# Kernel tuning notes

Hardware: AMD Instinct MI355X
Metric: run time of the kernel (lower is better)

The kernel has to match this reference:

```python
import jax, jax.numpy as jnp
import numpy as np

N_NODES = 50000
N_EDGES = 800000
IN_FEATS = 128
N_HIDDEN = 128
N_CLASSES = 64


def setup_inputs() -> dict:
    key = jax.random.key(0)
    ks = jax.random.split(key, 12)
    x = jax.random.normal(ks[0], (N_NODES, IN_FEATS), dtype=jnp.float32)
    src = jax.random.randint(ks[1], (N_EDGES,), 0, N_NODES, dtype=jnp.int32)
    dst = jax.random.randint(ks[2], (N_EDGES,), 0, N_NODES, dtype=jnp.int32)
    dims = [(IN_FEATS, N_HIDDEN), (N_HIDDEN, N_HIDDEN), (N_HIDDEN, N_CLASSES)]
    inp = {"x": x, "src": src, "dst": dst}
    for i, (din, dout) in enumerate(dims):
        s = (2.0 / (din + dout)) ** 0.5  # xavier-ish init scale
        inp[f"Wself{i}"] = jax.random.normal(ks[3 + 3 * i], (din, dout), dtype=jnp.float32) * s
        inp[f"Wneigh{i}"] = jax.random.normal(ks[4 + 3 * i], (din, dout), dtype=jnp.float32) * s
        inp[f"b{i}"] = jnp.zeros((dout,), dtype=jnp.float32)
    return inp


def _sage_conv(h, src, dst, inv_deg, Wself, Wneigh, b):
    # mean aggregation over in-neighbors: gather on src, segment-sum on dst
    agg = jax.ops.segment_sum(h[src], dst, num_segments=N_NODES)  # [N, d]
    h_neigh = agg * inv_deg[:, None]
    return h @ Wself + h_neigh @ Wneigh + b


def reference(x, src, dst, Wself0, Wneigh0, b0, Wself1, Wneigh1, b1, Wself2, Wneigh2, b2):
    # in-degree (clamped to 1, matching DGL mean aggregator), shared across layers
    deg = jax.ops.segment_sum(jnp.ones((N_EDGES,), dtype=jnp.float32), dst, num_segments=N_NODES)
    inv_deg = 1.0 / jnp.maximum(deg, 1.0)
    # dropout is identity in eval mode
    h = _sage_conv(x, src, dst, inv_deg, Wself0, Wneigh0, b0)
    h = jax.nn.relu(h)
    h = _sage_conv(h, src, dst, inv_deg, Wself1, Wneigh1, b1)
    h = jax.nn.relu(h)
    h = _sage_conv(h, src, dst, inv_deg, Wself2, Wneigh2, b2)
    return h
```

## Files before the change

### kernel.cpp

```cpp
#include <hip/hip_runtime.h>

#define N_NODES 50000
#define N_EDGES 800000
#define NB_SCAN 196
#define NODES_PER_GRP 6250
#define BUCKET_CAP 131072

typedef unsigned short ushort_t;
typedef __attribute__((ext_vector_type(8))) short  short8v;
typedef __attribute__((ext_vector_type(4))) float  float4v;
typedef __attribute__((ext_vector_type(4))) unsigned short ushort4v;
typedef __attribute__((ext_vector_type(8))) unsigned short ushort8v;
typedef __attribute__((ext_vector_type(4))) int int4v;

__device__ __forceinline__ ushort_t f2bf(float f) {
    unsigned u = __float_as_uint(f);
    unsigned r = 0x7fffu + ((u >> 16) & 1u);
    return (ushort_t)((u + r) >> 16);
}
__device__ __forceinline__ float bf2f(ushort_t h) {
    return __uint_as_float((unsigned)h << 16);
}

__global__ __launch_bounds__(256) void cast_zero_k(const float* __restrict__ x,
                                                   ushort_t* __restrict__ xb,
                                                   int* __restrict__ deg,
                                                   int* __restrict__ bcur, int n4) {
    int i = blockIdx.x * 256 + threadIdx.x;
    if (i < n4) {
        float4 v = ((const float4*)x)[i];
        ushort4v h;
        h[0] = f2bf(v.x); h[1] = f2bf(v.y); h[2] = f2bf(v.z); h[3] = f2bf(v.w);
        ((ushort4v*)xb)[i] = h;
    }
    if (i < N_NODES) deg[i] = 0;
    if (i < 8) bcur[i] = 0;
}

__global__ __launch_bounds__(256) void bucket_k(const int4v* __restrict__ dst4,
                                                const int4v* __restrict__ src4,
                                                int* __restrict__ bcur,
                                                int2* __restrict__ buckets) {
    __shared__ int lcount[8];
    __shared__ int lbase[8];
    const int t = threadIdx.x, b = blockIdx.x;
    if (t < 8) lcount[t] = 0;
    __syncthreads();

    int4v d[4], s[4];
    const int base4 = b * 1024 + t;
#pragma unroll
    for (int i = 0; i < 4; ++i) {
        int idx = base4 + i * 256;
        if (idx < N_EDGES / 4) {
            d[i] = __builtin_nontemporal_load(dst4 + idx);
            s[i] = __builtin_nontemporal_load(src4 + idx);
        } else {
            d[i][0] = d[i][1] = d[i][2] = d[i][3] = -1;
            s[i][0] = s[i][1] = s[i][2] = s[i][3] = 0;
        }
    }
    int g[16], li[16];
#pragma unroll
    for (int i = 0; i < 4; ++i)
#pragma unroll
        for (int j = 0; j < 4; ++j) {
            int e = i * 4 + j;
            int dv = d[i][j];
            g[e] = (dv >= 0) ? (dv / NODES_PER_GRP) : -1;
            li[e] = (g[e] >= 0) ? atomicAdd(&lcount[g[e]], 1) : 0;
        }
    __syncthreads();
    if (t < 8) lbase[t] = atomicAdd(bcur + t, lcount[t]);
    __syncthreads();
#pragma unroll
    for (int i = 0; i < 4; ++i)
#pragma unroll
        for (int j = 0; j < 4; ++j) {
            int e = i * 4 + j;
            if (g[e] >= 0) {
                int pos = lbase[g[e]] + li[e];
                buckets[(size_t)g[e] * BUCKET_CAP + pos] = make_int2(d[i][j], s[i][j]);
            }
        }
}

__global__ __launch_bounds__(256) void deg_bucket_k(const int* __restrict__ bcur,
                                                    const int2* __restrict__ buckets,
                                                    int* __restrict__ deg) {
    const int grp = blockIdx.x & 7;
    const int cnt = bcur[grp];
    const int2* bk = buckets + (size_t)grp * BUCKET_CAP;
    const int stride = (gridDim.x >> 3) * 256;
    for (int i = (blockIdx.x >> 3) * 256 + threadIdx.x; i < cnt; i += stride) {
        atomicAdd(deg + bk[i].x, 1);
    }
}


__global__ __launch_bounds__(256) void block_sum_k(const int* __restrict__ deg,
                                                   int* __restrict__ bsum, int n) {
    __shared__ int s[256];
    int t = threadIdx.x, b = blockIdx.x;
    int i = b * 256 + t;
    s[t] = (i < n) ? deg[i] : 0;
    __syncthreads();
#pragma unroll
    for (int off = 128; off > 0; off >>= 1) {
        if (t < off) s[t] += s[t + off];
        __syncthreads();
    }
    if (t == 0) bsum[b] = s[0];
}

__global__ __launch_bounds__(256) void scan_bsum_k(const int* __restrict__ bsum,
                                                   int* __restrict__ boff,
                                                   int* __restrict__ rowptr_last, int nb) {
    __shared__ int s[256];
    int t = threadIdx.x;
    int v = (t < nb) ? bsum[t] : 0;
    s[t] = v;
    __syncthreads();
#pragma unroll
    for (int off = 1; off < 256; off <<= 1) {
        int u = (t >= off) ? s[t - off] : 0;
        __syncthreads();
        s[t] += u;
        __syncthreads();
    }
    if (t < nb) boff[t] = s[t] - v;
    if (t == 255) *rowptr_last = s[255];
}

__global__ __launch_bounds__(256) void write_rowptr_k(const int* __restrict__ deg,
                                                      const int* __restrict__ boff,
                                                      int* __restrict__ rowptr,
                                                      int* __restrict__ cursor,
                                                      float* __restrict__ inv, int n) {
    __shared__ int s[256];
    int t = threadIdx.x, b = blockIdx.x;
    int i = b * 256 + t;
    int d = (i < n) ? deg[i] : 0;
    s[t] = d;
    __syncthreads();
#pragma unroll
    for (int off = 1; off < 256; off <<= 1) {
        int u = (t >= off) ? s[t - off] : 0;
        __syncthreads();
        s[t] += u;
        __syncthreads();
    }
    if (i < n) {
        int r = boff[b] + s[t] - d;
        rowptr[i] = r;
        cursor[i] = r;
        inv[i] = 1.0f / fmaxf((float)d, 1.0f);
    }
}

__global__ __launch_bounds__(256) void scatter_bucket_k(const int* __restrict__ bcur,
                                                        const int2* __restrict__ buckets,
                                                        int* __restrict__ cursor,
                                                        int* __restrict__ csr) {
    const int grp = blockIdx.x & 7;
    const int cnt = bcur[grp];
    const int2* bk = buckets + (size_t)grp * BUCKET_CAP;
    const int stride = (gridDim.x >> 3) * 256;
    for (int i = (blockIdx.x >> 3) * 256 + threadIdx.x; i < cnt; i += stride) {
        int2 e = bk[i];
        csr[atomicAdd(cursor + e.x, 1)] = e.y;
    }
}

__global__ __launch_bounds__(256) void pack_all_k(const float* __restrict__ W0n, const float* __restrict__ W0s,
                                                  const float* __restrict__ W1n, const float* __restrict__ W1s,
                                                  const float* __restrict__ W2n, const float* __restrict__ W2s,
                                                  ushort_t* __restrict__ P) {
    int tid = blockIdx.x * 256 + threadIdx.x;
    const float* W; int dout; int base; int r;
    if      (tid < 2048)  { W = W0n; dout = 128; base = 0;     r = tid; }
    else if (tid < 4096)  { W = W0s; dout = 128; base = 16384; r = tid - 2048; }
    else if (tid < 6144)  { W = W1n; dout = 128; base = 32768; r = tid - 4096; }
    else if (tid < 8192)  { W = W1s; dout = 128; base = 49152; r = tid - 6144; }
    else if (tid < 9216)  { W = W2n; dout = 64;  base = 65536; r = tid - 8192; }
    else                  { W = W2s; dout = 64;  base = 73728; r = tid - 9216; }
    int lane = r & 63;
    int ks = (r >> 6) & 3;
    int nt = r >> 8;
    int col = nt * 16 + (lane & 15);
    int k0 = ks * 32 + ((lane >> 4) << 3);
    ushort_t* d = P + (size_t)base + (size_t)r * 8;
    ushort4v lo4, hi4;
#pragma unroll
    for (int j = 0; j < 4; ++j) lo4[j] = f2bf(W[(size_t)(k0 + j) * dout + col]);
#pragma unroll
    for (int j = 0; j < 4; ++j) hi4[j] = f2bf(W[(size_t)(k0 + 4 + j) * dout + col]);
    *(ushort4v*)d = lo4;
    *(ushort4v*)(d + 4) = hi4;
}

__global__ __launch_bounds__(256) void aggm_k(const ushort_t* __restrict__ h,
                                              const int* __restrict__ rowptr,
                                              const int* __restrict__ csr,
                                              const float* __restrict__ inv,
                                              ushort_t* __restrict__ m, int N) {
    int node = (blockIdx.x * 256 + threadIdx.x) >> 4;
    int c = threadIdx.x & 15;
    if (node >= N) return;
    int start = rowptr[node], end = rowptr[node + 1];

    const ushort8v* hp = (const ushort8v*)h;
    float a0[8] = {}, a1[8] = {}, a2[8] = {}, a3[8] = {};
    int j = start;
    for (; j + 3 < end; j += 4) {
        int u0 = csr[j], u1 = csr[j + 1], u2 = csr[j + 2], u3 = csr[j + 3];
        ushort8v w0 = hp[(size_t)u0 * 16 + c];
        ushort8v w1 = hp[(size_t)u1 * 16 + c];
        ushort8v w2 = hp[(size_t)u2 * 16 + c];
        ushort8v w3 = hp[(size_t)u3 * 16 + c];
#pragma unroll
        for (int k = 0; k < 8; ++k) {
            a0[k] += bf2f(w0[k]); a1[k] += bf2f(w1[k]);
            a2[k] += bf2f(w2[k]); a3[k] += bf2f(w3[k]);
        }
    }
    for (; j < end; ++j) {
        ushort8v w = hp[(size_t)csr[j] * 16 + c];
#pragma unroll
        for (int k = 0; k < 8; ++k) a0[k] += bf2f(w[k]);
    }
    float s = inv[node];
    ushort8v o;
#pragma unroll
    for (int k = 0; k < 8; ++k) o[k] = f2bf(((a0[k] + a1[k]) + (a2[k] + a3[k])) * s);
    ((ushort8v*)m)[(size_t)node * 16 + c] = o;
}

__global__ __launch_bounds__(256, 4) void fusedgemm_k(const ushort_t* __restrict__ H,
                                                      const ushort_t* __restrict__ M,
                                                      const short8v* __restrict__ Ws,
                                                      const short8v* __restrict__ Wn,
                                                      const float* __restrict__ bias,
                                                      ushort_t* __restrict__ Out, int N) {
    __shared__ ushort_t sm[2][64 * 128];
    char* sbH = (char*)sm[0];
    char* sbM = (char*)sm[1];
    const int bm = blockIdx.x * 64;
    const int t = threadIdx.x;
    const int w = t >> 6, l = t & 63;

    {
        const ushort8v* Hp = (const ushort8v*)H;
        const ushort8v* Mp = (const ushort8v*)M;
        ushort8v zeroV = {0, 0, 0, 0, 0, 0, 0, 0};
#pragma unroll
        for (int it = 0; it < 4; ++it) {
            int r = it * 16 + (t >> 4);
            int row = bm + r;
            int byte = (r * 256 + (t & 15) * 16) ^ ((r & 7) << 4);
            ushort8v vh = zeroV, vm = zeroV;
            if (row < N) {
                vh = Hp[(size_t)row * 16 + (t & 15)];
                vm = Mp[(size_t)row * 16 + (t & 15)];
            }
            *(ushort8v*)(sbH + byte) = vh;
            *(ushort8v*)(sbM + byte) = vm;
        }
    }
    __syncthreads();

    float bv[8];
#pragma unroll
    for (int nt = 0; nt < 8; ++nt) bv[nt] = bias[nt * 16 + (l & 15)];

    float4v acc[8] = {};
#pragma unroll
    for (int ks = 0; ks < 4; ++ks) {
        int r0 = w * 16 + (l & 15);
        int b0 = (r0 * 256 + ks * 64 + (l >> 4) * 16) ^ ((r0 & 7) << 4);
        short8v ah = *(const short8v*)(sbH + b0);
        short8v am = *(const short8v*)(sbM + b0);
#pragma unroll
        for (int nt = 0; nt < 8; ++nt) {
            short8v bs = Ws[(nt * 4 + ks) * 64 + l];
            short8v bn = Wn[(nt * 4 + ks) * 64 + l];
            acc[nt] = __builtin_amdgcn_mfma_f32_16x16x32_bf16(ah, bs, acc[nt], 0, 0, 0);
            acc[nt] = __builtin_amdgcn_mfma_f32_16x16x32_bf16(am, bn, acc[nt], 0, 0, 0);
        }
    }

#pragma unroll
    for (int i = 0; i < 4; ++i) {
        int row = bm + w * 16 + (l >> 4) * 4 + i;
        if (row < N) {
#pragma unroll
            for (int nt = 0; nt < 8; ++nt) {
                int col = nt * 16 + (l & 15);
                Out[(size_t)row * 128 + col] = f2bf(fmaxf(acc[nt][i] + bv[nt], 0.f));
            }
        }
    }
}

__global__ __launch_bounds__(256, 4) void dual64_k(const ushort_t* __restrict__ A,
                                                   const short8v* __restrict__ Wn,
                                                   const short8v* __restrict__ Ws,
                                                   const float* __restrict__ bias,
                                                   ushort_t* __restrict__ Z,
                                                   float* __restrict__ S, int N) {
    constexpr int NT = 4;
    __shared__ ushort_t Asm[64 * 128];
    char* sb = (char*)Asm;
    const int bm = blockIdx.x * 64;
    const int t = threadIdx.x;
    const int w = t >> 6, l = t & 63;

    {
        const ushort8v* Ap = (const ushort8v*)A;
        ushort8v zeroV = {0, 0, 0, 0, 0, 0, 0, 0};
#pragma unroll
        for (int it = 0; it < 4; ++it) {
            int r = it * 16 + (t >> 4);
            int row = bm + r;
            ushort8v v = zeroV;
            if (row < N) v = Ap[(size_t)row * 16 + (t & 15)];
            int byte = (r * 256 + (t & 15) * 16) ^ ((r & 7) << 4);
            *(ushort8v*)(sb + byte) = v;
        }
    }
    __syncthreads();

    float bv[NT];
#pragma unroll
    for (int nt = 0; nt < NT; ++nt) bv[nt] = bias[nt * 16 + (l & 15)];

    float4v accS[NT] = {}, accN[NT] = {};
#pragma unroll
    for (int ks = 0; ks < 4; ++ks) {
        int r0 = w * 16 + (l & 15);
        int b0 = (r0 * 256 + ks * 64 + (l >> 4) * 16) ^ ((r0 & 7) << 4);
        short8v a = *(const short8v*)(sb + b0);
#pragma unroll
        for (int nt = 0; nt < NT; ++nt) {
            short8v bs = Ws[(nt * 4 + ks) * 64 + l];
            short8v bn = Wn[(nt * 4 + ks) * 64 + l];
            accS[nt] = __builtin_amdgcn_mfma_f32_16x16x32_bf16(a, bs, accS[nt], 0, 0, 0);
            accN[nt] = __builtin_amdgcn_mfma_f32_16x16x32_bf16(a, bn, accN[nt], 0, 0, 0);
        }
    }

#pragma unroll
    for (int i = 0; i < 4; ++i) {
        int row = bm + w * 16 + (l >> 4) * 4 + i;
        if (row < N) {
#pragma unroll
            for (int nt = 0; nt < NT; ++nt) {
                int col = nt * 16 + (l & 15);
                S[(size_t)row * 64 + col] = accS[nt][i] + bv[nt];
                Z[(size_t)row * 64 + col] = f2bf(accN[nt][i]);
            }
        }
    }
}

__global__ __launch_bounds__(256) void agg64_k(const ushort_t* __restrict__ z,
                                               const int* __restrict__ rowptr,
                                               const int* __restrict__ csr,
                                               const float* __restrict__ inv,
                                               float* __restrict__ out, int N) {
    int node = (blockIdx.x * 256 + threadIdx.x) >> 3;
    int c = threadIdx.x & 7;
    if (node >= N) return;
    int start = rowptr[node], end = rowptr[node + 1];

    const ushort8v* zp = (const ushort8v*)z;
    float a0[8] = {}, a1[8] = {}, a2[8] = {}, a3[8] = {};
    int j = start;
    for (; j + 3 < end; j += 4) {
        int u0 = csr[j], u1 = csr[j + 1], u2 = csr[j + 2], u3 = csr[j + 3];
        ushort8v w0 = zp[(size_t)u0 * 8 + c];
        ushort8v w1 = zp[(size_t)u1 * 8 + c];
        ushort8v w2 = zp[(size_t)u2 * 8 + c];
        ushort8v w3 = zp[(size_t)u3 * 8 + c];
#pragma unroll
        for (int k = 0; k < 8; ++k) {
            a0[k] += bf2f(w0[k]); a1[k] += bf2f(w1[k]);
            a2[k] += bf2f(w2[k]); a3[k] += bf2f(w3[k]);
        }
    }
    for (; j < end; ++j) {
        ushort8v w = zp[(size_t)csr[j] * 8 + c];
#pragma unroll
        for (int k = 0; k < 8; ++k) a0[k] += bf2f(w[k]);
    }
    float s = inv[node];
    float* op = out + (size_t)node * 64 + c * 8;
    float4 o0 = *(float4*)op;
    float4 o1 = *(float4*)(op + 4);
    o0.x += ((a0[0] + a1[0]) + (a2[0] + a3[0])) * s;
    o0.y += ((a0[1] + a1[1]) + (a2[1] + a3[1])) * s;
    o0.z += ((a0[2] + a1[2]) + (a2[2] + a3[2])) * s;
    o0.w += ((a0[3] + a1[3]) + (a2[3] + a3[3])) * s;
    o1.x += ((a0[4] + a1[4]) + (a2[4] + a3[4])) * s;
    o1.y += ((a0[5] + a1[5]) + (a2[5] + a3[5])) * s;
    o1.z += ((a0[6] + a1[6]) + (a2[6] + a3[6])) * s;
    o1.w += ((a0[7] + a1[7]) + (a2[7] + a3[7])) * s;
    *(float4*)op = o0;
    *(float4*)(op + 4) = o1;
}


extern "C" void kernel_launch(void* const* d_in, const int* in_sizes, int n_in,
                              void* d_out, int out_size, void* d_ws, size_t ws_size,
                              hipStream_t stream) {
    const float* x       = (const float*)d_in[0];
    const int*   src     = (const int*)d_in[1];
    const int*   dst     = (const int*)d_in[2];
    const float* Wself0  = (const float*)d_in[3];
    const float* Wneigh0 = (const float*)d_in[4];
    const float* b0      = (const float*)d_in[5];
    const float* Wself1  = (const float*)d_in[6];
    const float* Wneigh1 = (const float*)d_in[7];
    const float* b1      = (const float*)d_in[8];
    const float* Wself2  = (const float*)d_in[9];
    const float* Wneigh2 = (const float*)d_in[10];
    const float* b2      = (const float*)d_in[11];
    float* out = (float*)d_out;

    char* ws = (char*)d_ws;
    size_t off = 0;
    auto alloc = [&](size_t bytes) -> void* {
        void* p = ws + off;
        off += (bytes + 255) & ~(size_t)255;
        return p;
    };
    int*      deg     = (int*)alloc((size_t)N_NODES * 4);
    float*    inv     = (float*)alloc((size_t)N_NODES * 4);
    int*      rowptr  = (int*)alloc((size_t)(N_NODES + 1) * 4);
    int*      cursor  = (int*)alloc((size_t)N_NODES * 4);
    int*      csr     = (int*)alloc((size_t)N_EDGES * 4);
    int*      bsum    = (int*)alloc((size_t)NB_SCAN * 4);
    int*      boff    = (int*)alloc((size_t)NB_SCAN * 4);
    int*      bcur    = (int*)alloc((size_t)8 * 4);
    int2*     buckets = (int2*)alloc((size_t)8 * BUCKET_CAP * 8);
    ushort_t* packW   = (ushort_t*)alloc((size_t)81920 * 2);
    ushort_t* xb      = (ushort_t*)alloc((size_t)N_NODES * 128 * 2);
    ushort_t* mbuf    = (ushort_t*)alloc((size_t)N_NODES * 128 * 2);
    ushort_t* h1      = (ushort_t*)alloc((size_t)N_NODES * 128 * 2);
    ushort_t* h2      = (ushort_t*)alloc((size_t)N_NODES * 128 * 2);
    ushort_t* z64     = (ushort_t*)alloc((size_t)N_NODES * 64 * 2);

    dim3 b256(256);
    const int gemmBlocks   = (N_NODES + 63) / 64;
    const int aggmBlocks   = (N_NODES * 16 + 255) / 256;
    const int agg64Blocks  = (N_NODES * 8 + 255) / 256;
    const int castBlocks   = (N_NODES * 32 + 255) / 256;
    const int bucketBlocks = (N_EDGES + 4095) / 4096;

    cast_zero_k<<<castBlocks, b256, 0, stream>>>(x, xb, deg, bcur, N_NODES * 32);
    bucket_k<<<bucketBlocks, b256, 0, stream>>>((const int4v*)dst, (const int4v*)src, bcur, buckets);
    deg_bucket_k<<<512, b256, 0, stream>>>(bcur, buckets, deg);
    block_sum_k<<<NB_SCAN, b256, 0, stream>>>(deg, bsum, N_NODES);
    scan_bsum_k<<<1, b256, 0, stream>>>(bsum, boff, rowptr + N_NODES, NB_SCAN);
    write_rowptr_k<<<NB_SCAN, b256, 0, stream>>>(deg, boff, rowptr, cursor, inv, N_NODES);
    scatter_bucket_k<<<512, b256, 0, stream>>>(bcur, buckets, cursor, csr);

    pack_all_k<<<40, b256, 0, stream>>>(Wneigh0, Wself0, Wneigh1, Wself1, Wneigh2, Wself2, packW);
    const short8v* pN0 = (const short8v*)(packW);
    const short8v* pS0 = (const short8v*)(packW + 16384);
    const short8v* pN1 = (const short8v*)(packW + 32768);
    const short8v* pS1 = (const short8v*)(packW + 49152);
    const short8v* pN2 = (const short8v*)(packW + 65536);
    const short8v* pS2 = (const short8v*)(packW + 73728);

    aggm_k<<<aggmBlocks, b256, 0, stream>>>(xb, rowptr, csr, inv, mbuf, N_NODES);
    fusedgemm_k<<<gemmBlocks, b256, 0, stream>>>(xb, mbuf, pS0, pN0, b0, h1, N_NODES);

    aggm_k<<<aggmBlocks, b256, 0, stream>>>(h1, rowptr, csr, inv, mbuf, N_NODES);
    fusedgemm_k<<<gemmBlocks, b256, 0, stream>>>(h1, mbuf, pS1, pN1, b1, h2, N_NODES);

    dual64_k<<<gemmBlocks, b256, 0, stream>>>(h2, pN2, pS2, b2, z64, out, N_NODES);
    agg64_k<<<agg64Blocks, b256, 0, stream>>>(z64, rowptr, csr, inv, out, N_NODES);
}
```

Baseline: 220.5 us.

## Fuse preprocessing kernels to cut launches in CSR build and weight packing

Merges weight packing into the cast kernel via extra blocks, folds degree counting into the bucketing kernel with global atomics on dst, and combines the block-offset scan with the rowptr write so each block redoes the small 196-entry scan. This removes three kernel launches and the extra pass over the bucket buffer. In exchange, bucket_k now issues 800k scattered global atomics inline, and every rowptr block repeats the tiny scan.

```diff
diff --git a/kernel.cpp b/kernel.cpp
--- a/kernel.cpp
+++ b/kernel.cpp
@@ -5,6 +5,7 @@
 #define NB_SCAN 196
 #define NODES_PER_GRP 6250
 #define BUCKET_CAP 131072
+#define CAST_BLOCKS 6250
 
 typedef unsigned short ushort_t;
 typedef __attribute__((ext_vector_type(8))) short  short8v;
@@ -22,161 +23,28 @@
     return __uint_as_float((unsigned)h << 16);
 }
 
-__global__ __launch_bounds__(256) void cast_zero_k(const float* __restrict__ x,
+__global__ __launch_bounds__(256) void cast_pack_k(const float* __restrict__ x,
                                                    ushort_t* __restrict__ xb,
                                                    int* __restrict__ deg,
-                                                   int* __restrict__ bcur, int n4) {
-    int i = blockIdx.x * 256 + threadIdx.x;
-    if (i < n4) {
-        float4 v = ((const float4*)x)[i];
-        ushort4v h;
-        h[0] = f2bf(v.x); h[1] = f2bf(v.y); h[2] = f2bf(v.z); h[3] = f2bf(v.w);
-        ((ushort4v*)xb)[i] = h;
-    }
-    if (i < N_NODES) deg[i] = 0;
-    if (i < 8) bcur[i] = 0;
-}
-
-__global__ __launch_bounds__(256) void bucket_k(const int4v* __restrict__ dst4,
-                                                const int4v* __restrict__ src4,
-                                                int* __restrict__ bcur,
-                                                int2* __restrict__ buckets) {
-    __shared__ int lcount[8];
-    __shared__ int lbase[8];
-    const int t = threadIdx.x, b = blockIdx.x;
-    if (t < 8) lcount[t] = 0;
-    __syncthreads();
-
-    int4v d[4], s[4];
-    const int base4 = b * 1024 + t;
-#pragma unroll
-    for (int i = 0; i < 4; ++i) {
-        int idx = base4 + i * 256;
-        if (idx < N_EDGES / 4) {
-            d[i] = __builtin_nontemporal_load(dst4 + idx);
-            s[i] = __builtin_nontemporal_load(src4 + idx);
-        } else {
-            d[i][0] = d[i][1] = d[i][2] = d[i][3] = -1;
-            s[i][0] = s[i][1] = s[i][2] = s[i][3] = 0;
-        }
-    }
-    int g[16], li[16];
-#pragma unroll
-    for (int i = 0; i < 4; ++i)
-#pragma unroll
-        for (int j = 0; j < 4; ++j) {
-            int e = i * 4 + j;
-            int dv = d[i][j];
-            g[e] = (dv >= 0) ? (dv / NODES_PER_GRP) : -1;
-            li[e] = (g[e] >= 0) ? atomicAdd(&lcount[g[e]], 1) : 0;
-        }
-    __syncthreads();
-    if (t < 8) lbase[t] = atomicAdd(bcur + t, lcount[t]);
-    __syncthreads();
-#pragma unroll
-    for (int i = 0; i < 4; ++i)
-#pragma unroll
-        for (int j = 0; j < 4; ++j) {
-            int e = i * 4 + j;
-            if (g[e] >= 0) {
-                int pos = lbase[g[e]] + li[e];
-                buckets[(size_t)g[e] * BUCKET_CAP + pos] = make_int2(d[i][j], s[i][j]);
-            }
-        }
-}
-
-__global__ __launch_bounds__(256) void deg_bucket_k(const int* __restrict__ bcur,
-                                                    const int2* __restrict__ buckets,
-                                                    int* __restrict__ deg) {
-    const int grp = blockIdx.x & 7;
-    const int cnt = bcur[grp];
-    const int2* bk = buckets + (size_t)grp * BUCKET_CAP;
-    const int stride = (gridDim.x >> 3) * 256;
-    for (int i = (blockIdx.x >> 3) * 256 + threadIdx.x; i < cnt; i += stride) {
-        atomicAdd(deg + bk[i].x, 1);
-    }
-}
-
-
-__global__ __launch_bounds__(256) void block_sum_k(const int* __restrict__ deg,
-                                                   int* __restrict__ bsum, int n) {
-    __shared__ int s[256];
-    int t = threadIdx.x, b = blockIdx.x;
-    int i = b * 256 + t;
-    s[t] = (i < n) ? deg[i] : 0;
-    __syncthreads();
-#pragma unroll
-    for (int off = 128; off > 0; off >>= 1) {
-        if (t < off) s[t] += s[t + off];
-        __syncthreads();
-    }
-    if (t == 0) bsum[b] = s[0];
-}
-
-__global__ __launch_bounds__(256) void scan_bsum_k(const int* __restrict__ bsum,
-                                                   int* __restrict__ boff,
-                                                   int* __restrict__ rowptr_last, int nb) {
-    __shared__ int s[256];
-    int t = threadIdx.x;
-    int v = (t < nb) ? bsum[t] : 0;
-    s[t] = v;
-    __syncthreads();
-#pragma unroll
-    for (int off = 1; off < 256; off <<= 1) {
-        int u = (t >= off) ? s[t - off] : 0;
-        __syncthreads();
-        s[t] += u;
-        __syncthreads();
-    }
-    if (t < nb) boff[t] = s[t] - v;
-    if (t == 255) *rowptr_last = s[255];
-}
-
-__global__ __launch_bounds__(256) void write_rowptr_k(const int* __restrict__ deg,
-                                                      const int* __restrict__ boff,
-                                                      int* __restrict__ rowptr,
-                                                      int* __restrict__ cursor,
-                                                      float* __restrict__ inv, int n) {
-    __shared__ int s[256];
-    int t = threadIdx.x, b = blockIdx.x;
-    int i = b * 256 + t;
-    int d = (i < n) ? deg[i] : 0;
-    s[t] = d;
-    __syncthreads();
-#pragma unroll
-    for (int off = 1; off < 256; off <<= 1) {
-        int u = (t >= off) ? s[t - off] : 0;
-        __syncthreads();
-        s[t] += u;
-        __syncthreads();
-    }
-    if (i < n) {
-        int r = boff[b] + s[t] - d;
-        rowptr[i] = r;
-        cursor[i] = r;
-        inv[i] = 1.0f / fmaxf((float)d, 1.0f);
-    }
-}
-
-__global__ __launch_bounds__(256) void scatter_bucket_k(const int* __restrict__ bcur,
-                                                        const int2* __restrict__ buckets,
-                                                        int* __restrict__ cursor,
-                                                        int* __restrict__ csr) {
-    const int grp = blockIdx.x & 7;
-    const int cnt = bcur[grp];
-    const int2* bk = buckets + (size_t)grp * BUCKET_CAP;
-    const int stride = (gridDim.x >> 3) * 256;
-    for (int i = (blockIdx.x >> 3) * 256 + threadIdx.x; i < cnt; i += stride) {
-        int2 e = bk[i];
-        csr[atomicAdd(cursor + e.x, 1)] = e.y;
-    }
-}
-
-__global__ __launch_bounds__(256) void pack_all_k(const float* __restrict__ W0n, const float* __restrict__ W0s,
-                                                  const float* __restrict__ W1n, const float* __restrict__ W1s,
-                                                  const float* __restrict__ W2n, const float* __restrict__ W2s,
-                                                  ushort_t* __restrict__ P) {
-    int tid = blockIdx.x * 256 + threadIdx.x;
+                                                   int* __restrict__ bcur,
+                                                   const float* __restrict__ W0n, const float* __restrict__ W0s,
+                                                   const float* __restrict__ W1n, const float* __restrict__ W1s,
+                                                   const float* __restrict__ W2n, const float* __restrict__ W2s,
+                                                   ushort_t* __restrict__ P) {
+    const int b = blockIdx.x, t = threadIdx.x;
+    if (b < CAST_BLOCKS) {
+        int i = b * 256 + t;
+        if (i < N_NODES * 32) {
+            float4 v = ((const float4*)x)[i];
+            ushort4v h;
+            h[0] = f2bf(v.x); h[1] = f2bf(v.y); h[2] = f2bf(v.z); h[3] = f2bf(v.w);
+            ((ushort4v*)xb)[i] = h;
+        }
+        if (i < N_NODES) deg[i] = 0;
+        if (i < 8) bcur[i] = 0;
+        return;
+    }
+    int tid = (b - CAST_BLOCKS) * 256 + t;
     const float* W; int dout; int base; int r;
     if      (tid < 2048)  { W = W0n; dout = 128; base = 0;     r = tid; }
     else if (tid < 4096)  { W = W0s; dout = 128; base = 16384; r = tid - 2048; }
@@ -197,6 +65,125 @@
     for (int j = 0; j < 4; ++j) hi4[j] = f2bf(W[(size_t)(k0 + 4 + j) * dout + col]);
     *(ushort4v*)d = lo4;
     *(ushort4v*)(d + 4) = hi4;
+}
+
+__global__ __launch_bounds__(256) void bucket_k(const int4v* __restrict__ dst4,
+                                                const int4v* __restrict__ src4,
+                                                int* __restrict__ bcur,
+                                                int2* __restrict__ buckets,
+                                                int* __restrict__ deg) {
+    __shared__ int lcount[8];
+    __shared__ int lbase[8];
+    const int t = threadIdx.x, b = blockIdx.x;
+    if (t < 8) lcount[t] = 0;
+    __syncthreads();
+
+    int4v d[4], s[4];
+    const int base4 = b * 1024 + t;
+#pragma unroll
+    for (int i = 0; i < 4; ++i) {
+        int idx = base4 + i * 256;
+        if (idx < N_EDGES / 4) {
+            d[i] = __builtin_nontemporal_load(dst4 + idx);
+            s[i] = __builtin_nontemporal_load(src4 + idx);
+        } else {
+            d[i][0] = d[i][1] = d[i][2] = d[i][3] = -1;
+            s[i][0] = s[i][1] = s[i][2] = s[i][3] = 0;
+        }
+    }
+    int g[16], li[16];
+#pragma unroll
+    for (int i = 0; i < 4; ++i)
+#pragma unroll
+        for (int j = 0; j < 4; ++j) {
+            int e = i * 4 + j;
+            int dv = d[i][j];
+            g[e] = (dv >= 0) ? (dv / NODES_PER_GRP) : -1;
+            li[e] = (g[e] >= 0) ? atomicAdd(&lcount[g[e]], 1) : 0;
+            if (dv >= 0) atomicAdd(deg + dv, 1);
+        }
+    __syncthreads();
+    if (t < 8) lbase[t] = atomicAdd(bcur + t, lcount[t]);
+    __syncthreads();
+#pragma unroll
+    for (int i = 0; i < 4; ++i)
+#pragma unroll
+        for (int j = 0; j < 4; ++j) {
+            int e = i * 4 + j;
+            if (g[e] >= 0) {
+                int pos = lbase[g[e]] + li[e];
+                buckets[(size_t)g[e] * BUCKET_CAP + pos] = make_int2(d[i][j], s[i][j]);
+            }
+        }
+}
+
+__global__ __launch_bounds__(256) void block_sum_k(const int* __restrict__ deg,
+                                                   int* __restrict__ bsum, int n) {
+    __shared__ int s[256];
+    int t = threadIdx.x, b = blockIdx.x;
+    int i = b * 256 + t;
+    s[t] = (i < n) ? deg[i] : 0;
+    __syncthreads();
+#pragma unroll
+    for (int off = 128; off > 0; off >>= 1) {
+        if (t < off) s[t] += s[t + off];
+        __syncthreads();
+    }
+    if (t == 0) bsum[b] = s[0];
+}
+
+__global__ __launch_bounds__(256) void rowptr_fused_k(const int* __restrict__ deg,
+                                                      const int* __restrict__ bsum,
+                                                      int* __restrict__ rowptr,
+                                                      int* __restrict__ cursor,
+                                                      float* __restrict__ inv) {
+    __shared__ int sb[256];
+    __shared__ int s[256];
+    const int t = threadIdx.x, b = blockIdx.x;
+    int v = (t < NB_SCAN) ? bsum[t] : 0;
+    sb[t] = v;
+    __syncthreads();
+#pragma unroll
+    for (int off = 1; off < 256; off <<= 1) {
+        int u = (t >= off) ? sb[t - off] : 0;
+        __syncthreads();
+        sb[t] += u;
+        __syncthreads();
+    }
+    const int boffb = (b == 0) ? 0 : sb[b - 1];
+    if (b == NB_SCAN - 1 && t == 0) rowptr[N_NODES] = sb[NB_SCAN - 1];
+
+    int i = b * 256 + t;
+    int d = (i < N_NODES) ? deg[i] : 0;
+    s[t] = d;
+    __syncthreads();
+#pragma unroll
+    for (int off = 1; off < 256; off <<= 1) {
+        int u = (t >= off) ? s[t - off] : 0;
+        __syncthreads();
+        s[t] += u;
+        __syncthreads();
+    }
+    if (i < N_NODES) {
+        int r = boffb + s[t] - d;
+        rowptr[i] = r;
+        cursor[i] = r;
+        inv[i] = 1.0f / fmaxf((float)d, 1.0f);
+    }
+}
+
+__global__ __launch_bounds__(256) void scatter_bucket_k(const int* __restrict__ bcur,
+                                                        const int2* __restrict__ buckets,
+                                                        int* __restrict__ cursor,
+                                                        int* __restrict__ csr) {
+    const int grp = blockIdx.x & 7;
+    const int cnt = bcur[grp];
+    const int2* bk = buckets + (size_t)grp * BUCKET_CAP;
+    const int stride = (gridDim.x >> 3) * 256;
+    for (int i = (blockIdx.x >> 3) * 256 + threadIdx.x; i < cnt; i += stride) {
+        int2 e = bk[i];
+        csr[atomicAdd(cursor + e.x, 1)] = e.y;
+    }
 }
 
 __global__ __launch_bounds__(256) void aggm_k(const ushort_t* __restrict__ h,
@@ -440,7 +427,6 @@
     int*      cursor  = (int*)alloc((size_t)N_NODES * 4);
     int*      csr     = (int*)alloc((size_t)N_EDGES * 4);
     int*      bsum    = (int*)alloc((size_t)NB_SCAN * 4);
-    int*      boff    = (int*)alloc((size_t)NB_SCAN * 4);
     int*      bcur    = (int*)alloc((size_t)8 * 4);
     int2*     buckets = (int2*)alloc((size_t)8 * BUCKET_CAP * 8);
     ushort_t* packW   = (ushort_t*)alloc((size_t)81920 * 2);
@@ -454,18 +440,17 @@
     const int gemmBlocks   = (N_NODES + 63) / 64;
     const int aggmBlocks   = (N_NODES * 16 + 255) / 256;
     const int agg64Blocks  = (N_NODES * 8 + 255) / 256;
-    const int castBlocks   = (N_NODES * 32 + 255) / 256;
     const int bucketBlocks = (N_EDGES + 4095) / 4096;
 
-    cast_zero_k<<<castBlocks, b256, 0, stream>>>(x, xb, deg, bcur, N_NODES * 32);
-    bucket_k<<<bucketBlocks, b256, 0, stream>>>((const int4v*)dst, (const int4v*)src, bcur, buckets);
-    deg_bucket_k<<<512, b256, 0, stream>>>(bcur, buckets, deg);
+    cast_pack_k<<<CAST_BLOCKS + 40, b256, 0, stream>>>(x, xb, deg, bcur,
+                                                       Wneigh0, Wself0, Wneigh1, Wself1,
+                                                       Wneigh2, Wself2, packW);
+    bucket_k<<<bucketBlocks, b256, 0, stream>>>((const int4v*)dst, (const int4v*)src,
+                                                bcur, buckets, deg);
     block_sum_k<<<NB_SCAN, b256, 0, stream>>>(deg, bsum, N_NODES);
-    scan_bsum_k<<<1, b256, 0, stream>>>(bsum, boff, rowptr + N_NODES, NB_SCAN);
-    write_rowptr_k<<<NB_SCAN, b256, 0, stream>>>(deg, boff, rowptr, cursor, inv, N_NODES);
+    rowptr_fused_k<<<NB_SCAN, b256, 0, stream>>>(deg, bsum, rowptr, cursor, inv);
     scatter_bucket_k<<<512, b256, 0, stream>>>(bcur, buckets, cursor, csr);
 
-    pack_all_k<<<40, b256, 0, stream>>>(Wneigh0, Wself0, Wneigh1, Wself1, Wneigh2, Wself2, packW);
     const short8v* pN0 = (const short8v*)(packW);
     const short8v* pS0 = (const short8v*)(packW + 16384);
     const short8v* pN1 = (const short8v*)(packW + 32768);
```

New measurement: 215.4 us. 1.02x faster.
